# Optimization experiments

Hardware: AMD Instinct MI355X
Metric: run time of the kernel (lower is better)

The kernel has to match this reference:

```python
import jax, jax.numpy as jnp
import numpy as np

SCALAR_DIM = 64
VECTOR_DIM = 64
SPIN = 2
N_NODES = 100000
N_EDGES = 1600000


def setup_inputs() -> dict:
    key = jax.random.key(0)
    ks = jax.random.split(key, 10)
    in_dim = 2 * SCALAR_DIM + VECTOR_DIM + 3  # 195
    hid = SCALAR_DIM + VECTOR_DIM  # 128
    return {
        "h_s": jax.random.normal(ks[0], (N_NODES, SCALAR_DIM), jnp.float32),
        "h_v": jax.random.normal(ks[1], (N_NODES, VECTOR_DIM), jnp.float32),
        "pos": jax.random.normal(ks[2], (N_NODES, 2), jnp.float32),
        "orientation": jax.random.normal(ks[3], (N_NODES, 1), jnp.float32),
        "W1": jax.random.normal(ks[4], (in_dim, hid), jnp.float32) / np.sqrt(in_dim),
        "b1": jnp.zeros((hid,), jnp.float32),
        "W2": jax.random.normal(ks[5], (hid, hid), jnp.float32) / np.sqrt(hid),
        "b2": jnp.zeros((hid,), jnp.float32),
        "edge_index": jax.random.randint(ks[6], (2, N_EDGES), 0, N_NODES, jnp.int64 if jax.config.jax_enable_x64 else jnp.int32),
    }


def reference(h_s, h_v, pos, orientation, W1, b1, W2, b2, edge_index):
    src, dst = edge_index[0], edge_index[1]
    delta_pos = pos[src] - pos[dst]                      # [E, 2]
    dist = jnp.linalg.norm(delta_pos, axis=1, keepdims=True) + 1e-6
    phi_global = jnp.arctan2(delta_pos[:, 1], delta_pos[:, 0])
    alpha_i = orientation[dst, 0]                        # [E]
    delta_phi = phi_global - alpha_i
    geo_feat = jnp.concatenate(
        [dist,
         jnp.cos(SPIN * delta_phi)[:, None],
         jnp.sin(SPIN * delta_phi)[:, None]], axis=-1)   # [E, 3]
    beta_j = orientation[src, 0]
    rot_angle = (beta_j - alpha_i) * SPIN
    c, s = jnp.cos(rot_angle)[:, None], jnp.sin(rot_angle)[:, None]
    n_vecs = VECTOR_DIM // 2
    v_j = h_v[src].reshape(-1, n_vecs, 2)                # [E, n_vecs, 2]
    v_x = v_j[..., 0] * c - v_j[..., 1] * s
    v_y = v_j[..., 0] * s + v_j[..., 1] * c
    v_rot = jnp.stack([v_x, v_y], axis=-1).reshape(-1, VECTOR_DIM)
    msg_input = jnp.concatenate([h_s[src], h_s[dst], v_rot, geo_feat], axis=-1)
    raw_msg = jax.nn.silu(msg_input @ W1 + b1) @ W2 + b2  # [E, scalar+vector]
    msg_s = raw_msg[:, :SCALAR_DIM]
    msg_v = raw_msg[:, SCALAR_DIM:]
    out_s = jnp.zeros_like(h_s).at[dst].add(msg_s)
    out_v = jnp.zeros_like(h_v).at[dst].add(msg_v)
    return (h_s + out_s, h_v + out_v)
```

## Files before the change

### kernel.cpp

```cpp
#include <hip/hip_runtime.h>
#include <hip/hip_bf16.h>

#define NNODES   100000
#define NEDGES   1600000
#define HID      128
#define IN_DIM   195
#define MLD      232
#define HLD      136
#define EB       32
#define NTILES   (NEDGES / EB)

typedef __attribute__((ext_vector_type(8))) short short8;
typedef __attribute__((ext_vector_type(4))) float f32x4;

static __device__ __forceinline__ short bf16b(float x) {
  __hip_bfloat16 h = __float2bfloat16(x);
  short s;
  __builtin_memcpy(&s, &h, sizeof(short));
  return s;
}

__global__ void residual_kernel(const float* __restrict__ hs,
                                const float* __restrict__ hv,
                                float* __restrict__ out) {
  const int nf = NNODES * 64;
  const int lane = threadIdx.x & 63;
  const int wid = (blockIdx.x * blockDim.x + threadIdx.x) >> 6;
  const int nw = (gridDim.x * blockDim.x) >> 6;
  const int nchunk = (2 * nf) >> 8;
  for (int c = wid; c < nchunk; c += nw) {
    const int base = (c << 8) + lane;
    #pragma unroll
    for (int k = 0; k < 4; ++k) {
      const int idx = base + (k << 6);
      const float v = (idx < nf) ? hs[idx] : hv[idx - nf];
      atomicAdd(&out[idx], v);
    }
  }
}

__global__ __launch_bounds__(256, 2)
void edge_kernel(const float* __restrict__ hs, const float* __restrict__ hv,
                 const float* __restrict__ pos, const float* __restrict__ ori,
                 const float* __restrict__ W1, const float* __restrict__ b1,
                 const float* __restrict__ W2, const float* __restrict__ b2,
                 const int* __restrict__ eidx, float* __restrict__ out) {
  __shared__ __attribute__((aligned(16))) short sMsg0[EB][MLD];
  __shared__ __attribute__((aligned(16))) short sMsg1[EB][MLD];
  __shared__ __attribute__((aligned(16))) short sHid[EB][HLD];
  __shared__ int sDst[2][EB];

  const int tid = threadIdx.x;
  const int wc = tid >> 6;
  const int l  = tid & 63;
  const int lr = l & 15;
  const int lk = (l >> 4) * 8;
  const int crow = (l >> 4) * 4;

  short8 w1f[7][2], w2f[4][2];
  #pragma unroll
  for (int ks = 0; ks < 7; ++ks)
    #pragma unroll
    for (int ct = 0; ct < 2; ++ct) {
      const int col = wc * 32 + ct * 16 + lr;
      short8 f;
      #pragma unroll
      for (int j = 0; j < 8; ++j) {
        const int k = ks * 32 + lk + j;
        f[j] = (k < IN_DIM) ? bf16b(W1[k * HID + col]) : (short)0;
      }
      w1f[ks][ct] = f;
    }
  #pragma unroll
  for (int ks = 0; ks < 4; ++ks)
    #pragma unroll
    for (int ct = 0; ct < 2; ++ct) {
      const int col = wc * 32 + ct * 16 + lr;
      short8 f;
      #pragma unroll
      for (int j = 0; j < 8; ++j) {
        const int k = ks * 32 + lk + j;
        f[j] = bf16b(W2[k * HID + col]);
      }
      w2f[ks][ct] = f;
    }
  float bias1[2], bias2[2]; int cbase[2];
  #pragma unroll
  for (int ct = 0; ct < 2; ++ct) {
    const int col = wc * 32 + ct * 16 + lr;
    bias1[ct] = b1[col];
    bias2[ct] = b2[col];
    cbase[ct] = (col < 64) ? col : (NNODES * 64 + col - 64);
  }

  const int le = tid >> 3, p = tid & 7;
  for (int o = 195 + p; o < 224; o += 8) { sMsg0[le][o] = 0; sMsg1[le][o] = 0; }

  const float4* hs4 = reinterpret_cast<const float4*>(hs);
  const float4* hv4 = reinterpret_cast<const float4*>(hv);
  const float2* pos2 = reinterpret_cast<const float2*>(pos);
  const int G = gridDim.x;
  const int t0 = blockIdx.x;

  auto convert_store = [&](short (*msg)[MLD], int nbuf, int dstP,
                           float4 a0, float4 a1, float4 c0, float4 c1,
                           float4 v0, float4 v1, float2 ps, float2 pd,
                           float os, float od) {
    float dx = ps.x - pd.x, dy = ps.y - pd.y;
    float r2 = dx * dx + dy * dy;
    float dist = sqrtf(r2) + 1e-6f;
    float ir2 = (r2 > 0.f) ? (1.f / r2) : 0.f;
    float c2g = (r2 > 0.f) ? ((dx * dx - dy * dy) * ir2) : 1.f;
    float s2g = 2.f * dx * dy * ir2;
    float ca, sa, cb, sb;
    __sincosf(2.f * od, &sa, &ca);
    __sincosf(2.f * os, &sb, &cb);
    float c2 = c2g * ca + s2g * sa;
    float s2 = s2g * ca - c2g * sa;
    float cr = cb * ca + sb * sa;
    float sr = sb * ca - cb * sa;

    short8 m;
    m[0] = bf16b(a0.x); m[1] = bf16b(a0.y); m[2] = bf16b(a0.z); m[3] = bf16b(a0.w);
    m[4] = bf16b(a1.x); m[5] = bf16b(a1.y); m[6] = bf16b(a1.z); m[7] = bf16b(a1.w);
    *reinterpret_cast<short8*>(&msg[le][p * 8]) = m;
    m[0] = bf16b(c0.x); m[1] = bf16b(c0.y); m[2] = bf16b(c0.z); m[3] = bf16b(c0.w);
    m[4] = bf16b(c1.x); m[5] = bf16b(c1.y); m[6] = bf16b(c1.z); m[7] = bf16b(c1.w);
    *reinterpret_cast<short8*>(&msg[le][64 + p * 8]) = m;
    short8 mv;
    mv[0] = bf16b(v0.x * cr - v0.y * sr);
    mv[1] = bf16b(v0.x * sr + v0.y * cr);
    mv[2] = bf16b(v0.z * cr - v0.w * sr);
    mv[3] = bf16b(v0.z * sr + v0.w * cr);
    mv[4] = bf16b(v1.x * cr - v1.y * sr);
    mv[5] = bf16b(v1.x * sr + v1.y * cr);
    mv[6] = bf16b(v1.z * cr - v1.w * sr);
    mv[7] = bf16b(v1.z * sr + v1.w * cr);
    *reinterpret_cast<short8*>(&msg[le][128 + p * 8]) = mv;
    if (p == 0) {
      msg[le][192] = bf16b(dist);
      msg[le][193] = bf16b(c2);
      msg[le][194] = bf16b(s2);
      sDst[nbuf][le] = dstP;
    }
  };

  int srcN, dstN;
  {
    const int e = t0 * EB + le;
    srcN = eidx[e]; dstN = eidx[NEDGES + e];
  }
  {
    const int srcP = srcN, dstP = dstN;
    const int t1 = t0 + G;
    if (t1 < NTILES) {
      const int e = t1 * EB + le;
      srcN = eidx[e]; dstN = eidx[NEDGES + e];
    }
    convert_store(sMsg0, 0, dstP,
                  hs4[(size_t)srcP * 16 + p * 2], hs4[(size_t)srcP * 16 + p * 2 + 1],
                  hs4[(size_t)dstP * 16 + p * 2], hs4[(size_t)dstP * 16 + p * 2 + 1],
                  hv4[(size_t)srcP * 16 + p * 2], hv4[(size_t)srcP * 16 + p * 2 + 1],
                  pos2[srcP], pos2[dstP], ori[srcP], ori[dstP]);
  }
  __syncthreads();

  f32x4 accp[2][2];
  int4 d4p[2];
  int cur = 0;
  for (int t = t0; t < NTILES; t += G) {
    #pragma unroll
    for (int ks = 0; ks < 7; ++ks) {
      asm volatile("" : "+v"(w1f[ks][0]));
      asm volatile("" : "+v"(w1f[ks][1]));
    }
    #pragma unroll
    for (int ks = 0; ks < 4; ++ks) {
      asm volatile("" : "+v"(w2f[ks][0]));
      asm volatile("" : "+v"(w2f[ks][1]));
    }

    const int tn = t + G, tnn = t + 2 * G;
    const bool haveN = (tn < NTILES);
    short (*msgC)[MLD] = cur ? sMsg1 : sMsg0;
    short (*msgN)[MLD] = cur ? sMsg0 : sMsg1;

    float4 a0, a1, c0, c1, v0, v1; float2 ps, pd; float os, od;
    const int srcP = srcN, dstP = dstN;
    if (haveN) {
      a0 = hs4[(size_t)srcP * 16 + p * 2];
      a1 = hs4[(size_t)srcP * 16 + p * 2 + 1];
      c0 = hs4[(size_t)dstP * 16 + p * 2];
      c1 = hs4[(size_t)dstP * 16 + p * 2 + 1];
      v0 = hv4[(size_t)srcP * 16 + p * 2];
      v1 = hv4[(size_t)srcP * 16 + p * 2 + 1];
      ps = pos2[srcP]; pd = pos2[dstP];
      os = ori[srcP]; od = ori[dstP];
      if (tnn < NTILES) {
        const int e = tnn * EB + le;
        srcN = eidx[e]; dstN = eidx[NEDGES + e];
      }
    }

    if (t != t0) {
      #pragma unroll
      for (int rt = 0; rt < 2; ++rt)
        #pragma unroll
        for (int ct = 0; ct < 2; ++ct) {
          atomicAdd(&out[(size_t)d4p[rt].x * 64 + cbase[ct]], accp[rt][ct][0]);
          atomicAdd(&out[(size_t)d4p[rt].y * 64 + cbase[ct]], accp[rt][ct][1]);
          atomicAdd(&out[(size_t)d4p[rt].z * 64 + cbase[ct]], accp[rt][ct][2]);
          atomicAdd(&out[(size_t)d4p[rt].w * 64 + cbase[ct]], accp[rt][ct][3]);
        }
    }

    f32x4 acc[2][2] = {{{0,0,0,0},{0,0,0,0}},{{0,0,0,0},{0,0,0,0}}};
    #pragma unroll
    for (int ks = 0; ks < 7; ++ks) {
      #pragma unroll
      for (int rt = 0; rt < 2; ++rt) {
        short8 a = *reinterpret_cast<const short8*>(&msgC[rt * 16 + lr][ks * 32 + lk]);
        #pragma unroll
        for (int ct = 0; ct < 2; ++ct)
          acc[rt][ct] = __builtin_amdgcn_mfma_f32_16x16x32_bf16(a, w1f[ks][ct], acc[rt][ct], 0, 0, 0);
      }
    }
    #pragma unroll
    for (int rt = 0; rt < 2; ++rt)
      #pragma unroll
      for (int ct = 0; ct < 2; ++ct) {
        const int col = wc * 32 + ct * 16 + lr;
        #pragma unroll
        for (int j = 0; j < 4; ++j) {
          float x = acc[rt][ct][j] + bias1[ct];
          float h = __fdividef(x, 1.f + __expf(-x));
          sHid[rt * 16 + crow + j][col] = bf16b(h);
        }
      }
    __syncthreads();

    f32x4 acc2[2][2] = {{{0,0,0,0},{0,0,0,0}},{{0,0,0,0},{0,0,0,0}}};
    #pragma unroll
    for (int ks = 0; ks < 4; ++ks) {
      #pragma unroll
      for (int rt = 0; rt < 2; ++rt) {
        short8 a = *reinterpret_cast<const short8*>(&sHid[rt * 16 + lr][ks * 32 + lk]);
        #pragma unroll
        for (int ct = 0; ct < 2; ++ct)
          acc2[rt][ct] = __builtin_amdgcn_mfma_f32_16x16x32_bf16(a, w2f[ks][ct], acc2[rt][ct], 0, 0, 0);
      }
    }

    #pragma unroll
    for (int rt = 0; rt < 2; ++rt) {
      d4p[rt] = *reinterpret_cast<const int4*>(&sDst[cur][rt * 16 + crow]);
      #pragma unroll
      for (int ct = 0; ct < 2; ++ct) {
        accp[rt][ct][0] = acc2[rt][ct][0] + bias2[ct];
        accp[rt][ct][1] = acc2[rt][ct][1] + bias2[ct];
        accp[rt][ct][2] = acc2[rt][ct][2] + bias2[ct];
        accp[rt][ct][3] = acc2[rt][ct][3] + bias2[ct];
      }
    }

    if (haveN) {
      convert_store(msgN, cur ^ 1, dstP, a0, a1, c0, c1, v0, v1, ps, pd, os, od);
    }
    __syncthreads();
    cur ^= 1;
  }

  {
    #pragma unroll
    for (int rt = 0; rt < 2; ++rt)
      #pragma unroll
      for (int ct = 0; ct < 2; ++ct) {
        atomicAdd(&out[(size_t)d4p[rt].x * 64 + cbase[ct]], accp[rt][ct][0]);
        atomicAdd(&out[(size_t)d4p[rt].y * 64 + cbase[ct]], accp[rt][ct][1]);
        atomicAdd(&out[(size_t)d4p[rt].z * 64 + cbase[ct]], accp[rt][ct][2]);
        atomicAdd(&out[(size_t)d4p[rt].w * 64 + cbase[ct]], accp[rt][ct][3]);
      }
  }
}

extern "C" void kernel_launch(void* const* d_in, const int* in_sizes, int n_in,
                              void* d_out, int out_size, void* d_ws, size_t ws_size,
                              hipStream_t stream) {
  const float* hs  = (const float*)d_in[0];
  const float* hv  = (const float*)d_in[1];
  const float* pos = (const float*)d_in[2];
  const float* ori = (const float*)d_in[3];
  const float* W1  = (const float*)d_in[4];
  const float* b1  = (const float*)d_in[5];
  const float* W2  = (const float*)d_in[6];
  const float* b2  = (const float*)d_in[7];
  const int* eidx  = (const int*)d_in[8];
  float* out = (float*)d_out;

  hipLaunchKernelGGL(residual_kernel, dim3(2048), dim3(256), 0, stream,
                     hs, hv, out);
  hipLaunchKernelGGL(edge_kernel, dim3(512), dim3(256), 0, stream,
                     hs, hv, pos, ori, W1, b1, W2, b2, eidx, out);
}
```

Measured before the change: 809.0 us.

## Sort edges by destination and merge same-destination atomics before scatter

Adds a counting sort of edges by destination (histogram, three-stage scan, scatter) into workspace memory. Each block now processes a contiguous range of sorted tiles instead of a strided set, and the block-to-range mapping is interleaved. Runs of equal destinations within a lane's four output rows are pre-summed, so fewer global atomicAdds are issued and the remaining ones are more local. The sort costs several extra kernel launches and atomic passes on every call, and it only runs when the workspace is large enough.

```diff
diff --git a/kernel.cpp b/kernel.cpp
--- a/kernel.cpp
+++ b/kernel.cpp
@@ -9,6 +9,15 @@
 #define HLD      136
 #define EB       32
 #define NTILES   (NEDGES / EB)
+#define NBLK     512
+#define SCANB    1024
+#define NSCAN1   ((NNODES + SCANB - 1) / SCANB)
+
+#define OFS_CNT  (NSCAN1 * SCANB)
+#define BSUM_OFF ((size_t)OFS_CNT * 4)
+#define SRC_OFF  (BSUM_OFF + 512)
+#define DST_OFF  (SRC_OFF + (size_t)NEDGES * 4)
+#define WS_NEED  (DST_OFF + (size_t)NEDGES * 4)
 
 typedef __attribute__((ext_vector_type(8))) short short8;
 typedef __attribute__((ext_vector_type(4))) float f32x4;
@@ -18,6 +27,58 @@
   short s;
   __builtin_memcpy(&s, &h, sizeof(short));
   return s;
+}
+
+__global__ void hist_kernel(const int* __restrict__ eidx, int* __restrict__ ofs) {
+  int i = blockIdx.x * blockDim.x + threadIdx.x;
+  const int stride = gridDim.x * blockDim.x;
+  for (; i < NEDGES; i += stride) atomicAdd(&ofs[eidx[NEDGES + i]], 1);
+}
+
+__global__ __launch_bounds__(SCANB)
+void scan1_kernel(int* __restrict__ ofs, int* __restrict__ bsum) {
+  __shared__ int sh[SCANB];
+  const int t = threadIdx.x, i = blockIdx.x * SCANB + t;
+  const int x = ofs[i];
+  sh[t] = x; __syncthreads();
+  for (int off = 1; off < SCANB; off <<= 1) {
+    int v = (t >= off) ? sh[t - off] : 0;
+    __syncthreads();
+    sh[t] += v;
+    __syncthreads();
+  }
+  ofs[i] = sh[t] - x;
+  if (t == SCANB - 1) bsum[blockIdx.x] = sh[t];
+}
+
+__global__ void scan2_kernel(int* __restrict__ bsum) {
+  __shared__ int sh[128];
+  const int t = threadIdx.x;
+  const int x = (t < NSCAN1) ? bsum[t] : 0;
+  sh[t] = x; __syncthreads();
+  for (int off = 1; off < 128; off <<= 1) {
+    int v = (t >= off) ? sh[t - off] : 0;
+    __syncthreads();
+    sh[t] += v;
+    __syncthreads();
+  }
+  if (t < NSCAN1) bsum[t] = sh[t] - x;
+}
+
+__global__ void scan3_kernel(int* __restrict__ ofs, const int* __restrict__ bsum) {
+  const int i = blockIdx.x * blockDim.x + threadIdx.x;
+  ofs[i] += bsum[i >> 10];
+}
+
+__global__ void scatter_kernel(const int* __restrict__ eidx, int* __restrict__ ofs,
+                               int* __restrict__ ssrc, int* __restrict__ sdst) {
+  int i = blockIdx.x * blockDim.x + threadIdx.x;
+  const int stride = gridDim.x * blockDim.x;
+  for (; i < NEDGES; i += stride) {
+    const int s = eidx[i], d = eidx[NEDGES + i];
+    const int p = atomicAdd(&ofs[d], 1);
+    ssrc[p] = s; sdst[p] = d;
+  }
 }
 
 __global__ void residual_kernel(const float* __restrict__ hs,
@@ -44,7 +105,8 @@
                  const float* __restrict__ pos, const float* __restrict__ ori,
                  const float* __restrict__ W1, const float* __restrict__ b1,
                  const float* __restrict__ W2, const float* __restrict__ b2,
-                 const int* __restrict__ eidx, float* __restrict__ out) {
+                 const int* __restrict__ esrc, const int* __restrict__ edst,
+                 float* __restrict__ out) {
   __shared__ __attribute__((aligned(16))) short sMsg0[EB][MLD];
   __shared__ __attribute__((aligned(16))) short sMsg1[EB][MLD];
   __shared__ __attribute__((aligned(16))) short sHid[EB][HLD];
@@ -56,6 +118,12 @@
   const int lr = l & 15;
   const int lk = (l >> 4) * 8;
   const int crow = (l >> 4) * 4;
+
+  const int bid = blockIdx.x;
+  const int lb = ((bid & 7) << 6) + (bid >> 3);
+  const int q = NTILES / NBLK, r = NTILES % NBLK;
+  const int tstart = lb * q + (lb < r ? lb : r);
+  const int tend   = tstart + q + (lb < r ? 1 : 0);
 
   short8 w1f[7][2], w2f[4][2];
   #pragma unroll
@@ -99,8 +167,6 @@
   const float4* hs4 = reinterpret_cast<const float4*>(hs);
   const float4* hv4 = reinterpret_cast<const float4*>(hv);
   const float2* pos2 = reinterpret_cast<const float2*>(pos);
-  const int G = gridDim.x;
-  const int t0 = blockIdx.x;
 
   auto convert_store = [&](short (*msg)[MLD], int nbuf, int dstP,
                            float4 a0, float4 a1, float4 c0, float4 c1,
@@ -147,15 +213,14 @@
 
   int srcN, dstN;
   {
-    const int e = t0 * EB + le;
-    srcN = eidx[e]; dstN = eidx[NEDGES + e];
+    const int e = tstart * EB + le;
+    srcN = esrc[e]; dstN = edst[e];
   }
   {
     const int srcP = srcN, dstP = dstN;
-    const int t1 = t0 + G;
-    if (t1 < NTILES) {
-      const int e = t1 * EB + le;
-      srcN = eidx[e]; dstN = eidx[NEDGES + e];
+    if (tstart + 1 < tend) {
+      const int e = (tstart + 1) * EB + le;
+      srcN = esrc[e]; dstN = edst[e];
     }
     convert_store(sMsg0, 0, dstP,
                   hs4[(size_t)srcP * 16 + p * 2], hs4[(size_t)srcP * 16 + p * 2 + 1],
@@ -168,7 +233,7 @@
   f32x4 accp[2][2];
   int4 d4p[2];
   int cur = 0;
-  for (int t = t0; t < NTILES; t += G) {
+  for (int t = tstart; t < tend; ++t) {
     #pragma unroll
     for (int ks = 0; ks < 7; ++ks) {
       asm volatile("" : "+v"(w1f[ks][0]));
@@ -180,8 +245,7 @@
       asm volatile("" : "+v"(w2f[ks][1]));
     }
 
-    const int tn = t + G, tnn = t + 2 * G;
-    const bool haveN = (tn < NTILES);
+    const bool haveN = (t + 1 < tend);
     short (*msgC)[MLD] = cur ? sMsg1 : sMsg0;
     short (*msgN)[MLD] = cur ? sMsg0 : sMsg1;
 
@@ -196,22 +260,28 @@
       v1 = hv4[(size_t)srcP * 16 + p * 2 + 1];
       ps = pos2[srcP]; pd = pos2[dstP];
       os = ori[srcP]; od = ori[dstP];
-      if (tnn < NTILES) {
-        const int e = tnn * EB + le;
-        srcN = eidx[e]; dstN = eidx[NEDGES + e];
-      }
-    }
-
-    if (t != t0) {
-      #pragma unroll
-      for (int rt = 0; rt < 2; ++rt)
+      if (t + 2 < tend) {
+        const int e = (t + 2) * EB + le;
+        srcN = esrc[e]; dstN = edst[e];
+      }
+    }
+
+    if (t != tstart) {
+      #pragma unroll
+      for (int rt = 0; rt < 2; ++rt) {
+        const int d0 = d4p[rt].x, d1 = d4p[rt].y, d2 = d4p[rt].z, d3 = d4p[rt].w;
         #pragma unroll
         for (int ct = 0; ct < 2; ++ct) {
-          atomicAdd(&out[(size_t)d4p[rt].x * 64 + cbase[ct]], accp[rt][ct][0]);
-          atomicAdd(&out[(size_t)d4p[rt].y * 64 + cbase[ct]], accp[rt][ct][1]);
-          atomicAdd(&out[(size_t)d4p[rt].z * 64 + cbase[ct]], accp[rt][ct][2]);
-          atomicAdd(&out[(size_t)d4p[rt].w * 64 + cbase[ct]], accp[rt][ct][3]);
+          float s = accp[rt][ct][0]; int dp = d0;
+          if (d1 == dp) s += accp[rt][ct][1];
+          else { atomicAdd(&out[(size_t)dp * 64 + cbase[ct]], s); dp = d1; s = accp[rt][ct][1]; }
+          if (d2 == dp) s += accp[rt][ct][2];
+          else { atomicAdd(&out[(size_t)dp * 64 + cbase[ct]], s); dp = d2; s = accp[rt][ct][2]; }
+          if (d3 == dp) s += accp[rt][ct][3];
+          else { atomicAdd(&out[(size_t)dp * 64 + cbase[ct]], s); dp = d3; s = accp[rt][ct][3]; }
+          atomicAdd(&out[(size_t)dp * 64 + cbase[ct]], s);
         }
+      }
     }
 
     f32x4 acc[2][2] = {{{0,0,0,0},{0,0,0,0}},{{0,0,0,0},{0,0,0,0}}};
@@ -270,16 +340,20 @@
     cur ^= 1;
   }
 
-  {
-    #pragma unroll
-    for (int rt = 0; rt < 2; ++rt)
-      #pragma unroll
-      for (int ct = 0; ct < 2; ++ct) {
-        atomicAdd(&out[(size_t)d4p[rt].x * 64 + cbase[ct]], accp[rt][ct][0]);
-        atomicAdd(&out[(size_t)d4p[rt].y * 64 + cbase[ct]], accp[rt][ct][1]);
-        atomicAdd(&out[(size_t)d4p[rt].z * 64 + cbase[ct]], accp[rt][ct][2]);
-        atomicAdd(&out[(size_t)d4p[rt].w * 64 + cbase[ct]], accp[rt][ct][3]);
-      }
+  #pragma unroll
+  for (int rt = 0; rt < 2; ++rt) {
+    const int d0 = d4p[rt].x, d1 = d4p[rt].y, d2 = d4p[rt].z, d3 = d4p[rt].w;
+    #pragma unroll
+    for (int ct = 0; ct < 2; ++ct) {
+      float s = accp[rt][ct][0]; int dp = d0;
+      if (d1 == dp) s += accp[rt][ct][1];
+      else { atomicAdd(&out[(size_t)dp * 64 + cbase[ct]], s); dp = d1; s = accp[rt][ct][1]; }
+      if (d2 == dp) s += accp[rt][ct][2];
+      else { atomicAdd(&out[(size_t)dp * 64 + cbase[ct]], s); dp = d2; s = accp[rt][ct][2]; }
+      if (d3 == dp) s += accp[rt][ct][3];
+      else { atomicAdd(&out[(size_t)dp * 64 + cbase[ct]], s); dp = d3; s = accp[rt][ct][3]; }
+      atomicAdd(&out[(size_t)dp * 64 + cbase[ct]], s);
+    }
   }
 }
 
@@ -297,8 +371,24 @@
   const int* eidx  = (const int*)d_in[8];
   float* out = (float*)d_out;
 
-  hipLaunchKernelGGL(residual_kernel, dim3(2048), dim3(256), 0, stream,
-                     hs, hv, out);
-  hipLaunchKernelGGL(edge_kernel, dim3(512), dim3(256), 0, stream,
-                     hs, hv, pos, ori, W1, b1, W2, b2, eidx, out);
-}
+  const int* esrc = eidx;
+  const int* edst = eidx + NEDGES;
+
+  if (ws_size >= WS_NEED) {
+    int* ofs  = (int*)((char*)d_ws);
+    int* bsum = (int*)((char*)d_ws + BSUM_OFF);
+    int* ssrc = (int*)((char*)d_ws + SRC_OFF);
+    int* sdst = (int*)((char*)d_ws + DST_OFF);
+    hipMemsetAsync(ofs, 0, (size_t)OFS_CNT * 4, stream);
+    hipLaunchKernelGGL(hist_kernel, dim3(1024), dim3(256), 0, stream, eidx, ofs);
+    hipLaunchKernelGGL(scan1_kernel, dim3(NSCAN1), dim3(SCANB), 0, stream, ofs, bsum);
+    hipLaunchKernelGGL(scan2_kernel, dim3(1), dim3(128), 0, stream, bsum);
+    hipLaunchKernelGGL(scan3_kernel, dim3(OFS_CNT / 256), dim3(256), 0, stream, ofs, bsum);
+    hipLaunchKernelGGL(scatter_kernel, dim3(1024), dim3(256), 0, stream, eidx, ofs, ssrc, sdst);
+    esrc = ssrc; edst = sdst;
+  }
+
+  hipLaunchKernelGGL(residual_kernel, dim3(2048), dim3(256), 0, stream, hs, hv, out);
+  hipLaunchKernelGGL(edge_kernel, dim3(NBLK), dim3(256), 0, stream,
+                     hs, hv, pos, ori, W1, b1, W2, b2, esrc, edst, out);
+}
```

Measured after the change: 982.5 us. 21.4% more time.

## Stream pre-transposed bf16 weights from global memory to raise occupancy

Applied to the files above, without the earlier changes.

Adds a prep kernel that converts W1/W2 to transposed bf16 in the workspace. The edge kernel no longer keeps weight fragments pinned in registers and instead reloads them from global/L2 for each MFMA. Launch bounds go from 2 to 4 blocks per SM and the grid doubles to 1024 blocks. The aim is more resident waves to hide gather and atomic latency, at the cost of repeated weight loads on every tile.

```diff
diff --git a/kernel.cpp b/kernel.cpp
--- a/kernel.cpp
+++ b/kernel.cpp
@@ -5,10 +5,16 @@
 #define NEDGES   1600000
 #define HID      128
 #define IN_DIM   195
+#define KPAD     224
 #define MLD      232
 #define HLD      136
 #define EB       32
 #define NTILES   (NEDGES / EB)
+#define NBLK     1024
+
+#define W1T_ELEMS (HID * KPAD)
+#define W2T_ELEMS (HID * HID)
+#define WS_NEED   ((size_t)(W1T_ELEMS + W2T_ELEMS) * 2)
 
 typedef __attribute__((ext_vector_type(8))) short short8;
 typedef __attribute__((ext_vector_type(4))) float f32x4;
@@ -18,6 +24,20 @@
   short s;
   __builtin_memcpy(&s, &h, sizeof(short));
   return s;
+}
+
+__global__ void prep_weights(const float* __restrict__ W1,
+                             const float* __restrict__ W2,
+                             short* __restrict__ wt) {
+  const int i = blockIdx.x * blockDim.x + threadIdx.x;
+  if (i < W1T_ELEMS) {
+    const int col = i / KPAD, k = i % KPAD;
+    wt[i] = (k < IN_DIM) ? bf16b(W1[k * HID + col]) : (short)0;
+  } else if (i < W1T_ELEMS + W2T_ELEMS) {
+    const int j = i - W1T_ELEMS;
+    const int col = j >> 7, k = j & 127;
+    wt[i] = bf16b(W2[k * HID + col]);
+  }
 }
 
 __global__ void residual_kernel(const float* __restrict__ hs,
@@ -39,11 +59,11 @@
   }
 }
 
-__global__ __launch_bounds__(256, 2)
+__global__ __launch_bounds__(256, 4)
 void edge_kernel(const float* __restrict__ hs, const float* __restrict__ hv,
                  const float* __restrict__ pos, const float* __restrict__ ori,
-                 const float* __restrict__ W1, const float* __restrict__ b1,
-                 const float* __restrict__ W2, const float* __restrict__ b2,
+                 const short* __restrict__ wt,
+                 const float* __restrict__ b1, const float* __restrict__ b2,
                  const int* __restrict__ eidx, float* __restrict__ out) {
   __shared__ __attribute__((aligned(16))) short sMsg0[EB][MLD];
   __shared__ __attribute__((aligned(16))) short sMsg1[EB][MLD];
@@ -57,33 +77,13 @@
   const int lk = (l >> 4) * 8;
   const int crow = (l >> 4) * 4;
 
-  short8 w1f[7][2], w2f[4][2];
-  #pragma unroll
-  for (int ks = 0; ks < 7; ++ks)
-    #pragma unroll
-    for (int ct = 0; ct < 2; ++ct) {
-      const int col = wc * 32 + ct * 16 + lr;
-      short8 f;
-      #pragma unroll
-      for (int j = 0; j < 8; ++j) {
-        const int k = ks * 32 + lk + j;
-        f[j] = (k < IN_DIM) ? bf16b(W1[k * HID + col]) : (short)0;
-      }
-      w1f[ks][ct] = f;
-    }
-  #pragma unroll
-  for (int ks = 0; ks < 4; ++ks)
-    #pragma unroll
-    for (int ct = 0; ct < 2; ++ct) {
-      const int col = wc * 32 + ct * 16 + lr;
-      short8 f;
-      #pragma unroll
-      for (int j = 0; j < 8; ++j) {
-        const int k = ks * 32 + lk + j;
-        f[j] = bf16b(W2[k * HID + col]);
-      }
-      w2f[ks][ct] = f;
-    }
+  const short* w1t = wt;
+  const short* w2t = wt + W1T_ELEMS;
+  const short* w1b[2] = { &w1t[(wc * 32 + 0  + lr) * KPAD + lk],
+                          &w1t[(wc * 32 + 16 + lr) * KPAD + lk] };
+  const short* w2b[2] = { &w2t[(wc * 32 + 0  + lr) * HID + lk],
+                          &w2t[(wc * 32 + 16 + lr) * HID + lk] };
+
   float bias1[2], bias2[2]; int cbase[2];
   #pragma unroll
   for (int ct = 0; ct < 2; ++ct) {
@@ -169,17 +169,6 @@
   int4 d4p[2];
   int cur = 0;
   for (int t = t0; t < NTILES; t += G) {
-    #pragma unroll
-    for (int ks = 0; ks < 7; ++ks) {
-      asm volatile("" : "+v"(w1f[ks][0]));
-      asm volatile("" : "+v"(w1f[ks][1]));
-    }
-    #pragma unroll
-    for (int ks = 0; ks < 4; ++ks) {
-      asm volatile("" : "+v"(w2f[ks][0]));
-      asm volatile("" : "+v"(w2f[ks][1]));
-    }
-
     const int tn = t + G, tnn = t + 2 * G;
     const bool haveN = (tn < NTILES);
     short (*msgC)[MLD] = cur ? sMsg1 : sMsg0;
@@ -221,8 +210,10 @@
       for (int rt = 0; rt < 2; ++rt) {
         short8 a = *reinterpret_cast<const short8*>(&msgC[rt * 16 + lr][ks * 32 + lk]);
         #pragma unroll
-        for (int ct = 0; ct < 2; ++ct)
-          acc[rt][ct] = __builtin_amdgcn_mfma_f32_16x16x32_bf16(a, w1f[ks][ct], acc[rt][ct], 0, 0, 0);
+        for (int ct = 0; ct < 2; ++ct) {
+          short8 b = *reinterpret_cast<const short8*>(&w1b[ct][ks * 32]);
+          acc[rt][ct] = __builtin_amdgcn_mfma_f32_16x16x32_bf16(a, b, acc[rt][ct], 0, 0, 0);
+        }
       }
     }
     #pragma unroll
@@ -246,8 +237,10 @@
       for (int rt = 0; rt < 2; ++rt) {
         short8 a = *reinterpret_cast<const short8*>(&sHid[rt * 16 + lr][ks * 32 + lk]);
         #pragma unroll
-        for (int ct = 0; ct < 2; ++ct)
-          acc2[rt][ct] = __builtin_amdgcn_mfma_f32_16x16x32_bf16(a, w2f[ks][ct], acc2[rt][ct], 0, 0, 0);
+        for (int ct = 0; ct < 2; ++ct) {
+          short8 b = *reinterpret_cast<const short8*>(&w2b[ct][ks * 32]);
+          acc2[rt][ct] = __builtin_amdgcn_mfma_f32_16x16x32_bf16(a, b, acc2[rt][ct], 0, 0, 0);
+        }
       }
     }
 
@@ -270,17 +263,15 @@
     cur ^= 1;
   }
 
-  {
-    #pragma unroll
-    for (int rt = 0; rt < 2; ++rt)
-      #pragma unroll
-      for (int ct = 0; ct < 2; ++ct) {
-        atomicAdd(&out[(size_t)d4p[rt].x * 64 + cbase[ct]], accp[rt][ct][0]);
-        atomicAdd(&out[(size_t)d4p[rt].y * 64 + cbase[ct]], accp[rt][ct][1]);
-        atomicAdd(&out[(size_t)d4p[rt].z * 64 + cbase[ct]], accp[rt][ct][2]);
-        atomicAdd(&out[(size_t)d4p[rt].w * 64 + cbase[ct]], accp[rt][ct][3]);
-      }
-  }
+  #pragma unroll
+  for (int rt = 0; rt < 2; ++rt)
+    #pragma unroll
+    for (int ct = 0; ct < 2; ++ct) {
+      atomicAdd(&out[(size_t)d4p[rt].x * 64 + cbase[ct]], accp[rt][ct][0]);
+      atomicAdd(&out[(size_t)d4p[rt].y * 64 + cbase[ct]], accp[rt][ct][1]);
+      atomicAdd(&out[(size_t)d4p[rt].z * 64 + cbase[ct]], accp[rt][ct][2]);
+      atomicAdd(&out[(size_t)d4p[rt].w * 64 + cbase[ct]], accp[rt][ct][3]);
+    }
 }
 
 extern "C" void kernel_launch(void* const* d_in, const int* in_sizes, int n_in,
@@ -296,9 +287,11 @@
   const float* b2  = (const float*)d_in[7];
   const int* eidx  = (const int*)d_in[8];
   float* out = (float*)d_out;
-
-  hipLaunchKernelGGL(residual_kernel, dim3(2048), dim3(256), 0, stream,
-                     hs, hv, out);
-  hipLaunchKernelGGL(edge_kernel, dim3(512), dim3(256), 0, stream,
-                     hs, hv, pos, ori, W1, b1, W2, b2, eidx, out);
-}
+  short* wt = (short*)d_ws;
+
+  hipLaunchKernelGGL(prep_weights, dim3((W1T_ELEMS + W2T_ELEMS + 255) / 256), dim3(256),
+                     0, stream, W1, W2, wt);
+  hipLaunchKernelGGL(residual_kernel, dim3(2048), dim3(256), 0, stream, hs, hv, out);
+  hipLaunchKernelGGL(edge_kernel, dim3(NBLK), dim3(256), 0, stream,
+                     hs, hv, pos, ori, wt, b1, b2, eidx, out);
+}
```

After: 922.5 us. 14.0% more time.
